# Kernel optimization log

Hardware: AMD Instinct MI355X
Metric: run time of the kernel (lower is better)

## Reference

```python
import jax, jax.numpy as jnp
import numpy as np

DIM = 3072
NUM_HEADS = 24
HEAD_DIM = 128
INNER = NUM_HEADS * HEAD_DIM
EPS = 1e-5


def _layernorm(x, eps=EPS):
    # affine-free LayerNorm over the last (head_dim) axis
    mu = jnp.mean(x, axis=-1, keepdims=True)
    var = jnp.mean(jnp.square(x - mu), axis=-1, keepdims=True)
    return (x - mu) * jax.lax.rsqrt(var + eps)


def _rope_interleaved(x, cos, sin):
    # x: (B, S_img, H, D); cos/sin: (S_img, D//2). Non-neox (interleaved) style.
    x1 = x[..., 0::2]
    x2 = x[..., 1::2]
    c = cos[None, :, None, :]
    s = sin[None, :, None, :]
    o1 = x1 * c - x2 * s
    o2 = x2 * c + x1 * s
    return jnp.stack([o1, o2], axis=-1).reshape(x.shape)


def setup_inputs() -> dict:
    key = jax.random.key(0)
    ks = jax.random.split(key, 8)
    B, S_txt, S_img = 1, 256, 2048
    hidden_states = jax.random.normal(ks[0], (B, S_img, DIM), dtype=jnp.float32)
    encoder_hidden_states = jax.random.normal(ks[1], (B, S_txt, DIM), dtype=jnp.float32)
    cos = jax.random.uniform(ks[2], (S_img, HEAD_DIM // 2), dtype=jnp.float32)
    sin = jax.random.uniform(ks[3], (S_img, HEAD_DIM // 2), dtype=jnp.float32)
    Wqkv = jax.random.normal(ks[4], (DIM, 3 * INNER), dtype=jnp.float32) * (DIM ** -0.5)
    bqkv = jnp.zeros((3 * INNER,), dtype=jnp.float32)
    Wout = jax.random.normal(ks[5], (INNER, DIM), dtype=jnp.float32) * (INNER ** -0.5)
    bout = jnp.zeros((DIM,), dtype=jnp.float32)
    return {
        "hidden_states": hidden_states,
        "encoder_hidden_states": encoder_hidden_states,
        "cos": cos,
        "sin": sin,
        "Wqkv": Wqkv,
        "bqkv": bqkv,
        "Wout": Wout,
        "bout": bout,
        "text_seq_length": 256,
    }


def reference(hidden_states, encoder_hidden_states, cos, sin, Wqkv, bqkv, Wout, bout, text_seq_length):
    T = text_seq_length
    x = jnp.concatenate([encoder_hidden_states, hidden_states], axis=1)  # (B, S, dim)
    B, S, _ = x.shape
    qkv = x @ Wqkv + bqkv  # (B, S, 3*inner)
    q, k, v = jnp.split(qkv, 3, axis=-1)
    q = q.reshape(B, S, NUM_HEADS, HEAD_DIM)
    k = k.reshape(B, S, NUM_HEADS, HEAD_DIM)
    v = v.reshape(B, S, NUM_HEADS, HEAD_DIM)
    q = _layernorm(q)
    k = _layernorm(k)
    # partial RoPE: only on image-token slice
    q = jnp.concatenate([q[:, :T], _rope_interleaved(q[:, T:], cos, sin)], axis=1)
    k = jnp.concatenate([k[:, :T], _rope_interleaved(k[:, T:], cos, sin)], axis=1)
    scale = 1.0 / (HEAD_DIM ** 0.5)
    scores = jnp.einsum("bqhd,bkhd->bhqk", q, k) * scale
    probs = jax.nn.softmax(scores, axis=-1)
    out = jnp.einsum("bhqk,bkhd->bqhd", probs, v)
    out = out.reshape(B, S, INNER)
    out = out @ Wout + bout
    encoder_out = out[:, :T, :]
    hidden_out = out[:, T:, :]
    return (hidden_out, encoder_out)
```

## Files before the change

### kernel.cpp

```cpp
#include <hip/hip_runtime.h>

#define DIMC 3072
#define NH 24
#define HD 128
#define QKV_N 9216
#define S_TXT 256
#define S_IMG 2048
#define S_TOT 2304

typedef _Float16 f16x8 __attribute__((ext_vector_type(8)));
typedef _Float16 f16x4 __attribute__((ext_vector_type(4)));
typedef _Float16 f16x2 __attribute__((ext_vector_type(2)));
typedef float f32x4 __attribute__((ext_vector_type(4)));

#define MFMA(A, B, C) __builtin_amdgcn_mfma_f32_16x16x32_f16(A, B, C, 0, 0, 0)

#define QSCALE (0.08838834764831845f * 1.4426950408889634f)

__device__ __forceinline__ void gl2lds16(const _Float16* g, _Float16* l) {
    __builtin_amdgcn_global_load_lds(
        (const __attribute__((address_space(1))) unsigned int*)g,
        (__attribute__((address_space(3))) unsigned int*)l,
        16, 0, 0);
}

__global__ __launch_bounds__(256) void prep(
    const float* __restrict__ enc, const float* __restrict__ hid,
    const float* __restrict__ Wqkv, const float* __restrict__ Wout,
    _Float16* __restrict__ xh, _Float16* __restrict__ Wth,
    _Float16* __restrict__ W2h)
{
    __shared__ float T[64][68];
    const int bid = blockIdx.x;
    const int t = threadIdx.x;

    if (bid < S_TOT) {
        const int s = bid;
        const float* src = (s < S_TXT) ? enc + (size_t)s * DIMC
                                       : hid + (size_t)(s - S_TXT) * DIMC;
#pragma unroll
        for (int it = 0; it < 3; ++it) {
            const int i = (it * 256 + t) * 4;
            float4 v = *(const float4*)(src + i);
            f16x4 hv;
            hv.x = (_Float16)v.x; hv.y = (_Float16)v.y;
            hv.z = (_Float16)v.z; hv.w = (_Float16)v.w;
            *(f16x4*)(xh + (size_t)s * DIMC + i) = hv;
        }
        return;
    }

    const float* W;
    _Float16* Th;
    int n0, k0, ldw;
    if (bid < S_TOT + 144 * 48) {
        const int b2 = bid - S_TOT;
        W = Wqkv; Th = Wth; ldw = QKV_N;
        n0 = (b2 % 144) * 64; k0 = (b2 / 144) * 64;
    } else {
        const int b2 = bid - S_TOT - 144 * 48;
        W = Wout; Th = W2h; ldw = DIMC;
        n0 = (b2 % 48) * 64; k0 = (b2 / 48) * 64;
    }
    {
        const int r = t >> 2, c4 = (t & 3) * 16;
#pragma unroll
        for (int j = 0; j < 4; ++j) {
            float4 v = *(const float4*)(W + (size_t)(k0 + r) * ldw + n0 + c4 + j * 4);
            *(float4*)&T[r][c4 + j * 4] = v;
        }
    }
    __syncthreads();
    const int nr = t >> 2, kp = (t & 3) * 16;
    f16x8 hv0, hv1;
#pragma unroll
    for (int j = 0; j < 8; ++j) hv0[j] = (_Float16)T[kp + j][nr];
#pragma unroll
    for (int j = 0; j < 8; ++j) hv1[j] = (_Float16)T[kp + 8 + j][nr];
    _Float16* dh = Th + (size_t)(n0 + nr) * DIMC + k0 + kp;
    *(f16x8*)(dh) = hv0; *(f16x8*)(dh + 8) = hv1;
}

#define GEMM_DB_PRE()                                                         \
    const int cpx = (int)gridDim.x >> 3;                                      \
    const int wgid = (blockIdx.x & 7) * cpx + (blockIdx.x >> 3);              \
    const int bm = (wgid % 18) * 128;                                         \
    const int bn = (wgid / 18) * 128;                                         \
    const int tid = threadIdx.x;                                              \
    const int l = tid & 63, w = tid >> 6;                                     \
    const int wr = w >> 1, wc = w & 1;                                        \
    const int lr = l & 15, g = l >> 4;                                        \
    const int row0 = w * 16 + (l >> 2);                                       \
    const int swz = (((l & 3) ^ ((row0 >> 1) & 3)) * 8);                      \
    const _Float16* gA0 = Ah + (size_t)(bm + row0) * DIMC + swz;              \
    const _Float16* gA1 = Ah + (size_t)(bm + 64 + row0) * DIMC + swz;         \
    const _Float16* gB0 = Bh + (size_t)(bn + row0) * DIMC + swz;              \
    const _Float16* gB1 = Bh + (size_t)(bn + 64 + row0) * DIMC + swz;         \
    int aoff[4], boff[4];                                                     \
    _Pragma("unroll")                                                         \
    for (int i = 0; i < 4; ++i) {                                             \
        const int ra = wr * 64 + i * 16 + lr;                                 \
        const int rb = wc * 64 + i * 16 + lr;                                 \
        aoff[i] = ra * 32 + ((g ^ ((ra >> 1) & 3)) * 8);                      \
        boff[i] = rb * 32 + ((g ^ ((rb >> 1) & 3)) * 8);                      \
    }

#define GEMM_STAGE(dd, k0) do {                                               \
    gl2lds16(gA0 + (k0), &Ash[dd][(w * 16) * 32]);                            \
    gl2lds16(gA1 + (k0), &Ash[dd][(64 + w * 16) * 32]);                       \
    gl2lds16(gB0 + (k0), &Bsh[dd][(w * 16) * 32]);                            \
    gl2lds16(gB1 + (k0), &Bsh[dd][(64 + w * 16) * 32]);                       \
} while (0)

#define GEMM_DB_LOOP()                                                        \
    f32x4 acc[4][4] = {};                                                     \
    GEMM_STAGE(0, 0);                                                         \
    __syncthreads();                                                          \
    for (int T = 0; T < DIMC / 32; ++T) {                                     \
        const int d = T & 1;                                                  \
        if (T + 1 < DIMC / 32) GEMM_STAGE(d ^ 1, (T + 1) * 32);               \
        f16x8 bhf[4];                                                         \
        _Pragma("unroll")                                                     \
        for (int ni = 0; ni < 4; ++ni)                                        \
            bhf[ni] = *(const f16x8*)&Bsh[d][boff[ni]];                       \
        __builtin_amdgcn_s_setprio(1);                                        \
        _Pragma("unroll")                                                     \
        for (int mi = 0; mi < 4; ++mi) {                                      \
            f16x8 ahf = *(const f16x8*)&Ash[d][aoff[mi]];                     \
            _Pragma("unroll")                                                 \
            for (int ni = 0; ni < 4; ++ni)                                    \
                acc[mi][ni] = MFMA(ahf, bhf[ni], acc[mi][ni]);                \
        }                                                                     \
        __builtin_amdgcn_s_setprio(0);                                        \
        __syncthreads();                                                      \
    }

__global__ __launch_bounds__(256) void gemm_qkv(
    const _Float16* __restrict__ Ah, const _Float16* __restrict__ Bh,
    const float* __restrict__ bias,
    _Float16* __restrict__ Qh, _Float16* __restrict__ Kh,
    _Float16* __restrict__ Vt)
{
    __shared__ __attribute__((aligned(16))) _Float16 Ash[2][128 * 32];
    __shared__ __attribute__((aligned(16))) _Float16 Bsh[2][128 * 32];
    GEMM_DB_PRE()
    GEMM_DB_LOOP()

    const int nb = bn >> 7;
    const int typ = nb / NH;
    const int h = nb % NH;

    if (typ == 2) {
#pragma unroll
        for (int mi = 0; mi < 4; ++mi) {
            const int sbase = bm + wr * 64 + mi * 16 + g * 4;
#pragma unroll
            for (int ni = 0; ni < 4; ++ni) {
                const int col = wc * 64 + ni * 16 + lr;
                const float bv = bias[bn + col];
                f16x4 vv;
                vv.x = (_Float16)(acc[mi][ni][0] + bv);
                vv.y = (_Float16)(acc[mi][ni][1] + bv);
                vv.z = (_Float16)(acc[mi][ni][2] + bv);
                vv.w = (_Float16)(acc[mi][ni][3] + bv);
                *(f16x4*)&Vt[((size_t)h * HD + col) * S_TOT + sbase] = vv;
            }
        }
    } else {
        _Float16* dst = (typ ? Kh : Qh) + (size_t)h * S_TOT * HD;
#pragma unroll
        for (int mi = 0; mi < 4; ++mi)
#pragma unroll
            for (int ni = 0; ni < 4; ++ni) {
                const int col = wc * 64 + ni * 16 + lr;
                const float bv = bias[bn + col];
#pragma unroll
                for (int e = 0; e < 4; ++e) {
                    const int r = bm + wr * 64 + mi * 16 + g * 4 + e;
                    dst[(size_t)r * HD + col] = (_Float16)(acc[mi][ni][e] + bv);
                }
            }
    }
}

__global__ __launch_bounds__(256) void gemm_out(
    const _Float16* __restrict__ Ah, const _Float16* __restrict__ Bh,
    const float* __restrict__ bias, float* __restrict__ C)
{
    __shared__ __attribute__((aligned(16))) _Float16 Ash[2][128 * 32];
    __shared__ __attribute__((aligned(16))) _Float16 Bsh[2][128 * 32];
    GEMM_DB_PRE()
    GEMM_DB_LOOP()

#pragma unroll
    for (int mi = 0; mi < 4; ++mi)
#pragma unroll
        for (int ni = 0; ni < 4; ++ni) {
            const int cl = bn + wc * 64 + ni * 16 + lr;
            const float bv = bias[cl];
#pragma unroll
            for (int e = 0; e < 4; ++e) {
                const int r = bm + wr * 64 + mi * 16 + g * 4 + e;
                const int gr = (r < S_TXT) ? (S_IMG + r) : (r - S_TXT);
                C[(size_t)gr * DIMC + cl] = acc[mi][ni][e] + bv;
            }
        }
}

__global__ __launch_bounds__(256) void ln_rope_inplace(
    _Float16* __restrict__ Qh, _Float16* __restrict__ Kh,
    const float* __restrict__ cost, const float* __restrict__ sint)
{
    const int wave = threadIdx.x >> 6;
    const int lane = threadIdx.x & 63;
    const int task = blockIdx.x * 4 + wave;
    const int s = task / 48;
    const int rem = task % 48;
    const int qk = rem / 24;
    const int h = rem % 24;

    _Float16* p = (qk ? Kh : Qh) + ((size_t)h * S_TOT + s) * HD + lane * 2;
    f16x2 xv = *(const f16x2*)p;
    float x0 = (float)xv.x, x1 = (float)xv.y;

    float sum = x0 + x1;
    float sq = x0 * x0 + x1 * x1;
#pragma unroll
    for (int off = 1; off < 64; off <<= 1) {
        sum += __shfl_xor(sum, off, 64);
        sq  += __shfl_xor(sq, off, 64);
    }
    const float mu = sum * (1.0f / 128.0f);
    const float var = sq * (1.0f / 128.0f) - mu * mu;
    const float rstd = rsqrtf(var + 1e-5f);
    float y0 = (x0 - mu) * rstd;
    float y1 = (x1 - mu) * rstd;

    if (s >= S_TXT) {
        const int ip = s - S_TXT;
        const float c = cost[ip * 64 + lane];
        const float sn = sint[ip * 64 + lane];
        const float o0 = y0 * c - y1 * sn;
        const float o1 = y1 * c + y0 * sn;
        y0 = o0; y1 = o1;
    }
    if (qk == 0) { y0 *= QSCALE; y1 *= QSCALE; }

    f16x2 hv; hv.x = (_Float16)y0; hv.y = (_Float16)y1;
    *(f16x2*)p = hv;
}

__global__ __launch_bounds__(512) void attn_mfma(
    const _Float16* __restrict__ Qg, const _Float16* __restrict__ Kg,
    const _Float16* __restrict__ Vg, _Float16* __restrict__ aoh)
{
    __shared__ __attribute__((aligned(16))) _Float16 Ksh[4 * 64 * 32];
    __shared__ __attribute__((aligned(16))) _Float16 Vsh[128 * 64];
    __shared__ __attribute__((aligned(16))) _Float16 Pah[8 * 16 * 64];

    const int wgid = ((int)blockIdx.x & 7) * 54 + ((int)blockIdx.x >> 3);
    const int h = wgid / 18;
    const int q0 = (wgid % 18) * 128;
    const int tid = threadIdx.x;
    const int w = tid >> 6, l = tid & 63;
    const int lr = l & 15, g = l >> 4;

    const int qrow = q0 + w * 16 + lr;
    const _Float16* qb = Qg + ((size_t)h * S_TOT + qrow) * HD + g * 8;
    f16x8 qh[4];
#pragma unroll
    for (int db = 0; db < 4; ++db)
        qh[db] = *(const f16x8*)(qb + db * 32);

    f32x4 o[8] = {};
    float mrow = -3.0e38f, lrow = 0.0f;

    const int kxr = (lr >> 1) & 3;
    const int px  = lr & 7;
    int ksl[4];
#pragma unroll
    for (int db = 0; db < 4; ++db) ksl[db] = (g ^ kxr ^ db) * 8;
    const int vs0 = (g ^ px) * 8;
    const int vs1 = ((4 + g) ^ px) * 8;

    const int kkv = tid >> 3, kd = tid & 7;
    const int kdb = kd >> 1, kg0 = (kd & 1) * 2;
    const int kx = (kkv >> 1) & 3;
    const int kbase = kdb * 2048 + kkv * 32;
    const int vd = tid >> 2, vh = tid & 3;
    const int vx = vd & 7;
    const int vbase = vd * 64;
    const int vg0 = vh * 2;
    const _Float16* gK = Kg + ((size_t)h * S_TOT + kkv) * HD + kd * 16;
    const _Float16* gV = Vg + ((size_t)h * HD + vd) * S_TOT + vh * 16;

    uint4 rK0, rK1, rV0, rV1;
#define LOADKV(kv0) { \
    rK0 = *(const uint4*)(gK + (size_t)(kv0) * HD);     rK1 = *(const uint4*)(gK + (size_t)(kv0) * HD + 8); \
    rV0 = *(const uint4*)(gV + (kv0));                  rV1 = *(const uint4*)(gV + (kv0) + 8); }

    LOADKV(0);

    for (int kb = 0; kb < S_TOT / 64; ++kb) {
        __syncthreads();
        *(uint4*)&Ksh[kbase + (((kg0 + 0) ^ kx ^ kdb) * 8)] = rK0;
        *(uint4*)&Ksh[kbase + (((kg0 + 1) ^ kx ^ kdb) * 8)] = rK1;
        *(uint4*)&Vsh[vbase + (((vg0 + 0) ^ vx) * 8)] = rV0;
        *(uint4*)&Vsh[vbase + (((vg0 + 1) ^ vx) * 8)] = rV1;
        __syncthreads();
        if (kb + 1 < S_TOT / 64) LOADKV((kb + 1) * 64);

        f32x4 sT[4] = {};
        __builtin_amdgcn_s_setprio(1);
#pragma unroll
        for (int db = 0; db < 4; ++db)
#pragma unroll
            for (int mf = 0; mf < 4; ++mf) {
                f16x8 kf = *(const f16x8*)&Ksh[db * 2048 + (mf * 16 + lr) * 32 + ksl[db]];
                sT[mf] = MFMA(kf, qh[db], sT[mf]);
            }
        __builtin_amdgcn_s_setprio(0);

        float pm = -3.0e38f;
#pragma unroll
        for (int mf = 0; mf < 4; ++mf)
#pragma unroll
            for (int e = 0; e < 4; ++e)
                pm = fmaxf(pm, sT[mf][e]);
        pm = fmaxf(pm, __shfl_xor(pm, 16, 64));
        pm = fmaxf(pm, __shfl_xor(pm, 32, 64));

        if (__any(pm > mrow + 11.0f)) {
            const float mnew = fmaxf(mrow, pm);
            const float alpha = exp2f(mrow - mnew);
            lrow *= alpha;
            mrow = mnew;
            const float a0 = __shfl(alpha, g * 4 + 0, 64);
            const float a1 = __shfl(alpha, g * 4 + 1, 64);
            const float a2 = __shfl(alpha, g * 4 + 2, 64);
            const float a3 = __shfl(alpha, g * 4 + 3, 64);
#pragma unroll
            for (int df = 0; df < 8; ++df) {
                o[df][0] *= a0; o[df][1] *= a1; o[df][2] *= a2; o[df][3] *= a3;
            }
        }

        float rs = 0.0f;
        float ex_[4][4];
#pragma unroll
        for (int mf = 0; mf < 4; ++mf)
#pragma unroll
            for (int e = 0; e < 4; ++e) {
                const float pv = exp2f(sT[mf][e] - mrow);
                ex_[mf][e] = pv;
                rs += pv;
            }
        rs += __shfl_xor(rs, 16, 64);
        rs += __shfl_xor(rs, 32, 64);
        lrow += rs;

        {
            const int pbase = w * 1024 + lr * 64;
#pragma unroll
            for (int mf = 0; mf < 4; ++mf) {
                const int slot = ((mf * 2 + (g >> 1)) ^ px) * 8 + (g & 1) * 4;
                f16x2 t0; t0.x = (_Float16)ex_[mf][0]; t0.y = (_Float16)ex_[mf][1];
                f16x2 t1; t1.x = (_Float16)ex_[mf][2]; t1.y = (_Float16)ex_[mf][3];
                *(f16x2*)&Pah[pbase + slot]     = t0;
                *(f16x2*)&Pah[pbase + slot + 2] = t1;
            }
        }

        f16x8 pa0 = *(const f16x8*)&Pah[w * 1024 + lr * 64 + vs0];
        f16x8 pa1 = *(const f16x8*)&Pah[w * 1024 + lr * 64 + vs1];
        __builtin_amdgcn_s_setprio(1);
#pragma unroll
        for (int df = 0; df < 8; ++df) {
            f16x8 vf0 = *(const f16x8*)&Vsh[(df * 16 + lr) * 64 + vs0];
            f16x8 vf1 = *(const f16x8*)&Vsh[(df * 16 + lr) * 64 + vs1];
            o[df] = MFMA(pa0, vf0, o[df]);
            o[df] = MFMA(pa1, vf1, o[df]);
        }
        __builtin_amdgcn_s_setprio(0);
    }
#undef LOADKV

    const float inv = 1.0f / lrow;
    const float b0 = __shfl(inv, g * 4 + 0, 64);
    const float b1 = __shfl(inv, g * 4 + 1, 64);
    const float b2 = __shfl(inv, g * 4 + 2, 64);
    const float b3 = __shfl(inv, g * 4 + 3, 64);
    const float bb[4] = {b0, b1, b2, b3};
#pragma unroll
    for (int df = 0; df < 8; ++df)
#pragma unroll
        for (int e = 0; e < 4; ++e) {
            const int r = q0 + w * 16 + g * 4 + e;
            aoh[(size_t)r * DIMC + h * HD + df * 16 + lr] = (_Float16)(o[df][e] * bb[e]);
        }
}

extern "C" void kernel_launch(void* const* d_in, const int* in_sizes, int n_in,
                              void* d_out, int out_size, void* d_ws, size_t ws_size,
                              hipStream_t stream)
{
    const float* hid  = (const float*)d_in[0];
    const float* enc  = (const float*)d_in[1];
    const float* cost = (const float*)d_in[2];
    const float* sint = (const float*)d_in[3];
    const float* Wqkv = (const float*)d_in[4];
    const float* bqkv = (const float*)d_in[5];
    const float* Wout = (const float*)d_in[6];
    const float* bout = (const float*)d_in[7];
    float* out = (float*)d_out;

    char* ws = (char*)d_ws;
    _Float16* Qh  = (_Float16*)(ws + 0);
    _Float16* Kh  = (_Float16*)(ws + 14155776);
    _Float16* Vth = (_Float16*)(ws + 28311552);
    _Float16* aoh = (_Float16*)(ws + 42467328);
    _Float16* xh  = (_Float16*)(ws + 56623104);
    _Float16* Wth = (_Float16*)(ws + 70778880);
    _Float16* W2h = (_Float16*)(ws + 127401984);

    prep<<<S_TOT + 144 * 48 + 48 * 48, 256, 0, stream>>>(
        enc, hid, Wqkv, Wout, xh, Wth, W2h);
    gemm_qkv<<<18 * 72, 256, 0, stream>>>(xh, Wth, bqkv, Qh, Kh, Vth);
    ln_rope_inplace<<<(S_TOT * 48) / 4, 256, 0, stream>>>(Qh, Kh, cost, sint);
    attn_mfma<<<432, 512, 0, stream>>>(Qh, Kh, Vth, aoh);
    gemm_out<<<18 * 24, 256, 0, stream>>>(aoh, W2h, bout, out);
}
```

Baseline: 457.4 us.

## Restructure GEMM mainloop to prefetch two tiles ahead with explicit vmcnt waits

The double-buffered GEMM mainloop, which waited on every global load with a full __syncthreads, is replaced by a two-deep prefetch scheme in one LDS buffer. Each tile waits only for its own loads (vmcnt(4)), reads all A/B fragments into registers, then issues the next global->LDS stage into the just-freed buffer before running the MFMAs. This hides more global load latency behind compute in both the QKV and output GEMMs. It depends on hand-written s_waitcnt counts matching the number of outstanding loads, which is fragile if the compiler reorders memory ops.

```diff
diff --git a/kernel.cpp b/kernel.cpp
--- a/kernel.cpp
+++ b/kernel.cpp
@@ -81,7 +81,7 @@
     *(f16x8*)(dh) = hv0; *(f16x8*)(dh + 8) = hv1;
 }
 
-#define GEMM_DB_PRE()                                                         \
+#define GEMM_PRE()                                                            \
     const int cpx = (int)gridDim.x >> 3;                                      \
     const int wgid = (blockIdx.x & 7) * cpx + (blockIdx.x >> 3);              \
     const int bm = (wgid % 18) * 128;                                         \
@@ -103,37 +103,47 @@
         const int rb = wc * 64 + i * 16 + lr;                                 \
         aoff[i] = ra * 32 + ((g ^ ((ra >> 1) & 3)) * 8);                      \
         boff[i] = rb * 32 + ((g ^ ((rb >> 1) & 3)) * 8);                      \
-    }
-
-#define GEMM_STAGE(dd, k0) do {                                               \
-    gl2lds16(gA0 + (k0), &Ash[dd][(w * 16) * 32]);                            \
-    gl2lds16(gA1 + (k0), &Ash[dd][(64 + w * 16) * 32]);                       \
-    gl2lds16(gB0 + (k0), &Bsh[dd][(w * 16) * 32]);                            \
-    gl2lds16(gB1 + (k0), &Bsh[dd][(64 + w * 16) * 32]);                       \
+    }                                                                         \
+    f32x4 acc[4][4] = {};
+
+#define STAGE(base, k0) do {                                                  \
+    gl2lds16(gA0 + (k0), &L[(base) + (w * 16) * 32]);                         \
+    gl2lds16(gA1 + (k0), &L[(base) + (64 + w * 16) * 32]);                    \
+    gl2lds16(gB0 + (k0), &L[(base) + 4096 + (w * 16) * 32]);                  \
+    gl2lds16(gB1 + (k0), &L[(base) + 4096 + (64 + w * 16) * 32]);             \
 } while (0)
 
-#define GEMM_DB_LOOP()                                                        \
-    f32x4 acc[4][4] = {};                                                     \
-    GEMM_STAGE(0, 0);                                                         \
-    __syncthreads();                                                          \
-    for (int T = 0; T < DIMC / 32; ++T) {                                     \
-        const int d = T & 1;                                                  \
-        if (T + 1 < DIMC / 32) GEMM_STAGE(d ^ 1, (T + 1) * 32);               \
-        f16x8 bhf[4];                                                         \
+#define GEMM_TILE(ABASE, WAITSTR, DOSTAGE, SBASE, SK) do {                    \
+    asm volatile(WAITSTR ::: "memory");                                       \
+    __builtin_amdgcn_s_barrier();                                             \
+    f16x8 bhf_[4], ahf_[4];                                                   \
+    _Pragma("unroll")                                                         \
+    for (int ni = 0; ni < 4; ++ni)                                            \
+        bhf_[ni] = *(const f16x8*)&L[(ABASE) + 4096 + boff[ni]];              \
+    _Pragma("unroll")                                                         \
+    for (int mi = 0; mi < 4; ++mi)                                            \
+        ahf_[mi] = *(const f16x8*)&L[(ABASE) + aoff[mi]];                     \
+    asm volatile("s_waitcnt lgkmcnt(0)" ::: "memory");                        \
+    __builtin_amdgcn_s_barrier();                                             \
+    if (DOSTAGE) STAGE(SBASE, SK);                                            \
+    __builtin_amdgcn_s_setprio(1);                                            \
+    _Pragma("unroll")                                                         \
+    for (int mi = 0; mi < 4; ++mi)                                            \
         _Pragma("unroll")                                                     \
         for (int ni = 0; ni < 4; ++ni)                                        \
-            bhf[ni] = *(const f16x8*)&Bsh[d][boff[ni]];                       \
-        __builtin_amdgcn_s_setprio(1);                                        \
-        _Pragma("unroll")                                                     \
-        for (int mi = 0; mi < 4; ++mi) {                                      \
-            f16x8 ahf = *(const f16x8*)&Ash[d][aoff[mi]];                     \
-            _Pragma("unroll")                                                 \
-            for (int ni = 0; ni < 4; ++ni)                                    \
-                acc[mi][ni] = MFMA(ahf, bhf[ni], acc[mi][ni]);                \
-        }                                                                     \
-        __builtin_amdgcn_s_setprio(0);                                        \
-        __syncthreads();                                                      \
-    }
+            acc[mi][ni] = MFMA(ahf_[mi], bhf_[ni], acc[mi][ni]);              \
+    __builtin_amdgcn_s_setprio(0);                                            \
+} while (0)
+
+#define GEMM_LOOP()                                                           \
+    STAGE(0, 0);                                                              \
+    STAGE(8192, 32);                                                          \
+    for (int k0 = 0; k0 < DIMC - 64; k0 += 64) {                              \
+        GEMM_TILE(0,    "s_waitcnt vmcnt(4)", 1, 0,    k0 + 64);              \
+        GEMM_TILE(8192, "s_waitcnt vmcnt(4)", 1, 8192, k0 + 96);              \
+    }                                                                         \
+    GEMM_TILE(0,    "s_waitcnt vmcnt(4)", 0, 0, 0);                           \
+    GEMM_TILE(8192, "s_waitcnt vmcnt(0)", 0, 0, 0);
 
 __global__ __launch_bounds__(256) void gemm_qkv(
     const _Float16* __restrict__ Ah, const _Float16* __restrict__ Bh,
@@ -141,10 +151,9 @@
     _Float16* __restrict__ Qh, _Float16* __restrict__ Kh,
     _Float16* __restrict__ Vt)
 {
-    __shared__ __attribute__((aligned(16))) _Float16 Ash[2][128 * 32];
-    __shared__ __attribute__((aligned(16))) _Float16 Bsh[2][128 * 32];
-    GEMM_DB_PRE()
-    GEMM_DB_LOOP()
+    __shared__ __attribute__((aligned(16))) _Float16 L[16384];
+    GEMM_PRE()
+    GEMM_LOOP()
 
     const int nb = bn >> 7;
     const int typ = nb / NH;
@@ -187,10 +196,9 @@
     const _Float16* __restrict__ Ah, const _Float16* __restrict__ Bh,
     const float* __restrict__ bias, float* __restrict__ C)
 {
-    __shared__ __attribute__((aligned(16))) _Float16 Ash[2][128 * 32];
-    __shared__ __attribute__((aligned(16))) _Float16 Bsh[2][128 * 32];
-    GEMM_DB_PRE()
-    GEMM_DB_LOOP()
+    __shared__ __attribute__((aligned(16))) _Float16 L[16384];
+    GEMM_PRE()
+    GEMM_LOOP()
 
 #pragma unroll
     for (int mi = 0; mi < 4; ++mi)
```

New measurement: 415.2 us. 1.1x faster.
